# Optimization experiments

Hardware: AMD Instinct MI355X
Metric: run time of the kernel (lower is better)

Reference implementation:

```python
import jax, jax.numpy as jnp
import numpy as np

F_FIELDS = 39
VOCAB = 100000
EMB = 16
BATCH = 16384
H1, H2 = 32, 32


def setup_inputs() -> dict:
    key = jax.random.key(0)
    ks = jax.random.split(key, 10)
    Xi = jax.random.randint(ks[0], (BATCH, F_FIELDS, 1), 0, VOCAB, dtype=jnp.int64 if jax.config.jax_enable_x64 else jnp.int32).astype(jnp.int32)
    Xv = jax.random.uniform(ks[1], (BATCH, F_FIELDS), dtype=jnp.float32)
    # per-field embedding tables, stacked (all feature_sizes equal)
    emb1 = jax.random.normal(ks[2], (F_FIELDS, VOCAB, 1), dtype=jnp.float32)
    emb2 = jax.random.normal(ks[3], (F_FIELDS, VOCAB, EMB), dtype=jnp.float32)
    d_in = F_FIELDS * EMB
    W1 = jax.random.normal(ks[4], (d_in, H1), dtype=jnp.float32) / np.sqrt(d_in)
    b1 = jnp.zeros((H1,), dtype=jnp.float32)
    W2 = jax.random.normal(ks[5], (H1, H2), dtype=jnp.float32) / np.sqrt(H1)
    b2 = jnp.zeros((H2,), dtype=jnp.float32)
    bias = jax.random.normal(ks[6], (1,), dtype=jnp.float32)
    return {"Xi": Xi, "Xv": Xv, "emb1": emb1, "emb2": emb2,
            "W1": W1, "b1": b1, "W2": W2, "b2": b2, "bias": bias}


def reference(Xi, Xv, emb1, emb2, W1, b1, W2, b2, bias):
    B = Xi.shape[0]
    idx = Xi[:, :, 0]  # [B, F]
    # flatten per-field tables into one big table; offset indices by field
    off = idx + (jnp.arange(F_FIELDS, dtype=idx.dtype) * VOCAB)[None, :]  # [B, F]
    # first order: gather scalar per (b, f), scale by Xv
    first = emb1.reshape(F_FIELDS * VOCAB)[off] * Xv  # [B, F]
    # second order embeddings, scaled by Xv
    e2 = emb2.reshape(F_FIELDS * VOCAB, EMB)[off] * Xv[:, :, None]  # [B, F, E]
    s = jnp.sum(e2, axis=1)                      # [B, E]
    sq_sum = jnp.sum(e2 * e2, axis=1)            # [B, E]
    fm_second = 0.5 * (s * s - sq_sum)           # [B, E]
    # deep part on concatenated field embeddings
    deep_in = e2.reshape(B, F_FIELDS * EMB)
    h = jax.nn.relu(deep_in @ W1 + b1)
    h = jax.nn.relu(h @ W2 + b2)
    total = jnp.sum(first, axis=1) + jnp.sum(fm_second, axis=1) + jnp.sum(h, axis=1) + bias
    return total  # [B]
```

## Files before the change

kernel.cpp:

```cpp
#include <hip/hip_runtime.h>
#include <hip/hip_bf16.h>

#define F_FIELDS 39
#define VOCAB    100000
#define EMB      16
#define BATCH    16384
#define H1       32
#define H2       32
#define KSTEPS   20
#define KPW      5
#define FRAG_OFF (640*1024)

typedef __bf16 bf16x8 __attribute__((ext_vector_type(8)));
typedef float  f32x4  __attribute__((ext_vector_type(4)));

__global__ __launch_bounds__(256) void prep_kernel(
    const int*   __restrict__ Xi,  const float* __restrict__ Xv,
    const float* __restrict__ emb1,const float* __restrict__ W1,
    float* __restrict__ ws1, __bf16* __restrict__ wsfrag)
{
    const int blk = blockIdx.x;
    const int fld   = blk >> 5;
    const int chunk = blk & 31;
    const int t = threadIdx.x;
    const int b0 = chunk * 512 + t * 2;
    #pragma unroll
    for (int j = 0; j < 2; ++j) {
        int b = b0 + j;
        int idx  = Xi[b * F_FIELDS + fld];
        float xv = Xv[b * F_FIELDS + fld];
        ws1[b * F_FIELDS + fld] = emb1[fld * VOCAB + idx] * xv;
    }
    if (blk < 10) {
        int fidx = blk * 256 + t;
        if (fidx < KSTEPS * 2 * 64) {
            int lane = fidx & 63;
            int nh   = (fidx >> 6) & 1;
            int ks   = fidx >> 7;
            int k0   = ks * 32 + (lane >> 4) * 8;
            int n    = nh * 16 + (lane & 15);
            __bf16 vals[8];
            #pragma unroll
            for (int j = 0; j < 8; ++j) {
                int k = k0 + j;
                vals[j] = (k < F_FIELDS * EMB) ? (__bf16)W1[k * H1 + n] : (__bf16)0.0f;
            }
            *reinterpret_cast<bf16x8*>(&wsfrag[fidx * 8]) = *reinterpret_cast<const bf16x8*>(vals);
        }
    }
}

__global__ __launch_bounds__(256, 4) void deepfm_main(
    const int*   __restrict__ Xi,  const float* __restrict__ Xv,
    const float* __restrict__ emb2,
    const __bf16* __restrict__ wsW1, const float* __restrict__ ws1,
    const float* __restrict__ b1,  const float* __restrict__ W2,
    const float* __restrict__ b2,  const float* __restrict__ bias,
    float* __restrict__ out)
{
    __shared__ int   sXi[16 * F_FIELDS];
    __shared__ float sXv[16 * F_FIELDS];
    __shared__ float pacc[4][16][32];
    __shared__ float sbuf[4][16][16];
    __shared__ float qbuf[4][16];
    __shared__ float W2s[H1 * H2];
    __shared__ float hs[16][32];

    const int t    = threadIdx.x;
    const int h    = t >> 6;
    const int l    = t & 63;
    const int sloc = l & 15;
    const int q    = l >> 4;
    const int fpar = q >> 1;
    const int eoff = (q & 1) * 8;
    const int blk  = blockIdx.x;

    {
        const int base = blk * 16 * F_FIELDS;
        for (int i = t; i < 16 * F_FIELDS; i += 256) {
            sXi[i] = Xi[base + i];
            sXv[i] = Xv[base + i];
        }
    }
    reinterpret_cast<float4*>(W2s)[t] = reinterpret_cast<const float4*>(W2)[t];
    __syncthreads();

    float xvm[KPW];
    float4 g0[KPW], g1[KPW];
    #pragma unroll
    for (int ks = 0; ks < KPW; ++ks) {
        int f = 8 * ks + 2 * h + fpar;
        bool v = (f < F_FIELDS);
        int fi = v ? f : 0;
        int idx = sXi[sloc * F_FIELDS + fi];
        xvm[ks] = v ? sXv[sloc * F_FIELDS + fi] : 0.0f;
        const float4* rp = reinterpret_cast<const float4*>(emb2 + (fi * VOCAB + idx) * EMB + eoff);
        g0[ks] = rp[0];
        g1[ks] = rp[1];
    }

    const bf16x8* wsf = reinterpret_cast<const bf16x8*>(wsW1);
    f32x4 acc0 = {0.f,0.f,0.f,0.f}, acc1 = {0.f,0.f,0.f,0.f};
    float sa[8];
    float qq = 0.f;
    #pragma unroll
    for (int j = 0; j < 8; ++j) sa[j] = 0.f;

    #pragma unroll
    for (int ks = 0; ks < KPW; ++ks) {
        int kstep = 4 * ks + h;
        bf16x8 fr0 = wsf[(kstep * 2 + 0) * 64 + l];
        bf16x8 fr1 = wsf[(kstep * 2 + 1) * 64 + l];
        float xv = xvm[ks];
        float e[8] = { g0[ks].x*xv, g0[ks].y*xv, g0[ks].z*xv, g0[ks].w*xv,
                       g1[ks].x*xv, g1[ks].y*xv, g1[ks].z*xv, g1[ks].w*xv };
        bf16x8 a;
        #pragma unroll
        for (int j = 0; j < 8; ++j) {
            a[j] = (__bf16)e[j];
            sa[j] += e[j];
            qq   += e[j]*e[j];
        }
        acc0 = __builtin_amdgcn_mfma_f32_16x16x32_bf16(a, fr0, acc0, 0, 0, 0);
        acc1 = __builtin_amdgcn_mfma_f32_16x16x32_bf16(a, fr1, acc1, 0, 0, 0);
    }

    float sf[8];
    #pragma unroll
    for (int j = 0; j < 8; ++j) sf[j] = sa[j] + __shfl_xor(sa[j], 32);
    qq += __shfl_xor(qq, 32);
    qq += __shfl_xor(qq, 16);
    if (q < 2) {
        float4* srow = reinterpret_cast<float4*>(&sbuf[h][sloc][q * 8]);
        srow[0] = make_float4(sf[0], sf[1], sf[2], sf[3]);
        srow[1] = make_float4(sf[4], sf[5], sf[6], sf[7]);
    }
    if (l < 16) qbuf[h][sloc] = qq;

    float badd0 = (h == 0) ? b1[sloc]      : 0.f;
    float badd1 = (h == 0) ? b1[16 + sloc] : 0.f;
    #pragma unroll
    for (int r = 0; r < 4; ++r) {
        int row = q * 4 + r;
        pacc[h][row][sloc]      = acc0[r] + badd0;
        pacc[h][row][16 + sloc] = acc1[r] + badd1;
    }
    __syncthreads();

    {
        int ss = t >> 4, c = t & 15;
        hs[ss][c]      = fmaxf(pacc[0][ss][c]      + pacc[1][ss][c]      + pacc[2][ss][c]      + pacc[3][ss][c],      0.f);
        hs[ss][c + 16] = fmaxf(pacc[0][ss][c + 16] + pacc[1][ss][c + 16] + pacc[2][ss][c + 16] + pacc[3][ss][c + 16], 0.f);
    }
    __syncthreads();

    const int so = t >> 4;
    const int u  = t & 15;

    float sv = sbuf[0][so][u] + sbuf[1][so][u] + sbuf[2][so][u] + sbuf[3][so][u];
    float s2 = sv * sv;

    const float* w1row = ws1 + (blk * 16 + so) * F_FIELDS;
    float fo = w1row[u] + w1row[16 + u];
    if (u < 7) fo += w1row[32 + u];

    float a0 = b2[2 * u], a1 = b2[2 * u + 1];
    #pragma unroll
    for (int i = 0; i < H1; ++i) {
        float hv = hs[so][i];
        a0 += hv * W2s[i * H2 + 2 * u];
        a1 += hv * W2s[i * H2 + 2 * u + 1];
    }
    float psum = fmaxf(a0, 0.f) + fmaxf(a1, 0.f) + fo;

    psum += __shfl_xor(psum, 1);  s2 += __shfl_xor(s2, 1);
    psum += __shfl_xor(psum, 2);  s2 += __shfl_xor(s2, 2);
    psum += __shfl_xor(psum, 4);  s2 += __shfl_xor(s2, 4);
    psum += __shfl_xor(psum, 8);  s2 += __shfl_xor(s2, 8);

    if (u == 0) {
        float qtot = qbuf[0][so] + qbuf[1][so] + qbuf[2][so] + qbuf[3][so];
        out[blk * 16 + so] = psum + 0.5f * (s2 - qtot) + bias[0];
    }
}

extern "C" void kernel_launch(void* const* d_in, const int* in_sizes, int n_in,
                              void* d_out, int out_size, void* d_ws, size_t ws_size,
                              hipStream_t stream) {
    const int*   Xi   = (const int*)  d_in[0];
    const float* Xv   = (const float*)d_in[1];
    const float* emb1 = (const float*)d_in[2];
    const float* emb2 = (const float*)d_in[3];
    const float* W1   = (const float*)d_in[4];
    const float* b1   = (const float*)d_in[5];
    const float* W2   = (const float*)d_in[6];
    const float* b2   = (const float*)d_in[7];
    const float* bias = (const float*)d_in[8];
    float* out = (float*)d_out;

    float*  ws1    = (float*)d_ws;
    __bf16* wsfrag = (__bf16*)((float*)d_ws + FRAG_OFF);

    prep_kernel<<<F_FIELDS * 32, 256, 0, stream>>>(Xi, Xv, emb1, W1, ws1, wsfrag);
    deepfm_main<<<BATCH/16, 256, 0, stream>>>(Xi, Xv, emb2, wsfrag, ws1, b1, W2, b2, bias, out);
}
```

Before: 36.05 us.

## Transpose Xi field-major and split prep into separate emb1 gather kernels

Splits the old prep kernel into three: a W1 bf16 fragment swizzle, a shared-memory transpose of Xi into field-major order, and an emb1 gather that reads and writes coalesced field-major arrays. The Xv multiply for the first-order term moves into the main kernel, which reads the field-major gathered values. The aim is coalesced index reads and output writes, with blocks grouped by field for locality in the emb1 table. This adds two extra kernel launches and an extra global round trip for the transposed Xi, and the main kernel's first-order reads become strided across fields.

After: 37.48 us. 4.0% more time.

```diff
diff --git a/kernel.cpp b/kernel.cpp
--- a/kernel.cpp
+++ b/kernel.cpp
@@ -9,51 +9,73 @@
 #define H2       32
 #define KSTEPS   20
 #define KPW      5
-#define FRAG_OFF (640*1024)
+
+#define WS1E_OFF  0
+#define XIT_OFF   2555904
+#define FRAG_OFF  5111808
 
 typedef __bf16 bf16x8 __attribute__((ext_vector_type(8)));
 typedef float  f32x4  __attribute__((ext_vector_type(4)));
 
-__global__ __launch_bounds__(256) void prep_kernel(
-    const int*   __restrict__ Xi,  const float* __restrict__ Xv,
-    const float* __restrict__ emb1,const float* __restrict__ W1,
-    float* __restrict__ ws1, __bf16* __restrict__ wsfrag)
-{
+__global__ __launch_bounds__(256) void swizzle_w1_kernel(const float* __restrict__ W1,
+                                                         __bf16* __restrict__ ws)
+{
+    int fidx = blockIdx.x * 256 + threadIdx.x;
+    if (fidx >= KSTEPS * 2 * 64) return;
+    int lane = fidx & 63;
+    int nh   = (fidx >> 6) & 1;
+    int ks   = fidx >> 7;
+    int k0   = ks * 32 + (lane >> 4) * 8;
+    int n    = nh * 16 + (lane & 15);
+    __bf16 vals[8];
+    #pragma unroll
+    for (int j = 0; j < 8; ++j) {
+        int k = k0 + j;
+        vals[j] = (k < F_FIELDS * EMB) ? (__bf16)W1[k * H1 + n] : (__bf16)0.0f;
+    }
+    *reinterpret_cast<bf16x8*>(&ws[fidx * 8]) = *reinterpret_cast<const bf16x8*>(vals);
+}
+
+__global__ __launch_bounds__(256) void xi_transpose_kernel(const int* __restrict__ Xi,
+                                                           int* __restrict__ XiT)
+{
+    __shared__ int tile[F_FIELDS][65];
     const int blk = blockIdx.x;
-    const int fld   = blk >> 5;
-    const int chunk = blk & 31;
-    const int t = threadIdx.x;
-    const int b0 = chunk * 512 + t * 2;
-    #pragma unroll
-    for (int j = 0; j < 2; ++j) {
-        int b = b0 + j;
-        int idx  = Xi[b * F_FIELDS + fld];
-        float xv = Xv[b * F_FIELDS + fld];
-        ws1[b * F_FIELDS + fld] = emb1[fld * VOCAB + idx] * xv;
-    }
-    if (blk < 10) {
-        int fidx = blk * 256 + t;
-        if (fidx < KSTEPS * 2 * 64) {
-            int lane = fidx & 63;
-            int nh   = (fidx >> 6) & 1;
-            int ks   = fidx >> 7;
-            int k0   = ks * 32 + (lane >> 4) * 8;
-            int n    = nh * 16 + (lane & 15);
-            __bf16 vals[8];
-            #pragma unroll
-            for (int j = 0; j < 8; ++j) {
-                int k = k0 + j;
-                vals[j] = (k < F_FIELDS * EMB) ? (__bf16)W1[k * H1 + n] : (__bf16)0.0f;
-            }
-            *reinterpret_cast<bf16x8*>(&wsfrag[fidx * 8]) = *reinterpret_cast<const bf16x8*>(vals);
-        }
-    }
+    const int t   = threadIdx.x;
+    const int base = blk * 64 * F_FIELDS;
+    for (int i = t; i < 64 * F_FIELDS; i += 256) {
+        int s = i / F_FIELDS, f = i % F_FIELDS;
+        tile[f][s] = Xi[base + i];
+    }
+    __syncthreads();
+    for (int j = t; j < 64 * F_FIELDS; j += 256) {
+        int f = j >> 6, s = j & 63;
+        XiT[f * BATCH + blk * 64 + s] = tile[f][s];
+    }
+}
+
+__global__ __launch_bounds__(256) void emb1_prep_kernel(const int* __restrict__ XiT,
+                                                        const float* __restrict__ emb1,
+                                                        float* __restrict__ ws1e)
+{
+    const int b     = blockIdx.x;
+    const int sgrp  = b >> 3;
+    const int field = (b & 7) + 8 * (sgrp >> 5);
+    if (field >= F_FIELDS) return;
+    const int chunk = sgrp & 31;
+    const int g = chunk * 512 + threadIdx.x * 2;
+    int2 idx = *reinterpret_cast<const int2*>(&XiT[field * BATCH + g]);
+    const float* eb = emb1 + (size_t)field * VOCAB;
+    float2 o;
+    o.x = eb[idx.x];
+    o.y = eb[idx.y];
+    *reinterpret_cast<float2*>(&ws1e[field * BATCH + g]) = o;
 }
 
 __global__ __launch_bounds__(256, 4) void deepfm_main(
     const int*   __restrict__ Xi,  const float* __restrict__ Xv,
     const float* __restrict__ emb2,
-    const __bf16* __restrict__ wsW1, const float* __restrict__ ws1,
+    const __bf16* __restrict__ wsW1, const float* __restrict__ ws1e,
     const float* __restrict__ b1,  const float* __restrict__ W2,
     const float* __restrict__ b2,  const float* __restrict__ bias,
     float* __restrict__ out)
@@ -156,13 +178,15 @@
 
     const int so = t >> 4;
     const int u  = t & 15;
+    const int sg = blk * 16 + so;
 
     float sv = sbuf[0][so][u] + sbuf[1][so][u] + sbuf[2][so][u] + sbuf[3][so][u];
     float s2 = sv * sv;
 
-    const float* w1row = ws1 + (blk * 16 + so) * F_FIELDS;
-    float fo = w1row[u] + w1row[16 + u];
-    if (u < 7) fo += w1row[32 + u];
+    float fo = ws1e[u * BATCH + sg]        * sXv[so * F_FIELDS + u]
+             + ws1e[(u + 16) * BATCH + sg] * sXv[so * F_FIELDS + u + 16];
+    if (u < 7)
+        fo += ws1e[(u + 32) * BATCH + sg] * sXv[so * F_FIELDS + u + 32];
 
     float a0 = b2[2 * u], a1 = b2[2 * u + 1];
     #pragma unroll
@@ -180,7 +204,7 @@
 
     if (u == 0) {
         float qtot = qbuf[0][so] + qbuf[1][so] + qbuf[2][so] + qbuf[3][so];
-        out[blk * 16 + so] = psum + 0.5f * (s2 - qtot) + bias[0];
+        out[sg] = psum + 0.5f * (s2 - qtot) + bias[0];
     }
 }
 
@@ -198,9 +222,13 @@
     const float* bias = (const float*)d_in[8];
     float* out = (float*)d_out;
 
-    float*  ws1    = (float*)d_ws;
-    __bf16* wsfrag = (__bf16*)((float*)d_ws + FRAG_OFF);
-
-    prep_kernel<<<F_FIELDS * 32, 256, 0, stream>>>(Xi, Xv, emb1, W1, ws1, wsfrag);
-    deepfm_main<<<BATCH/16, 256, 0, stream>>>(Xi, Xv, emb2, wsfrag, ws1, b1, W2, b2, bias, out);
-}
+    char* wsb = (char*)d_ws;
+    float*  ws1e   = (float*)(wsb + WS1E_OFF);
+    int*    XiT    = (int*)  (wsb + XIT_OFF);
+    __bf16* wsfrag = (__bf16*)(wsb + FRAG_OFF);
+
+    swizzle_w1_kernel<<<(KSTEPS*2*64 + 255)/256, 256, 0, stream>>>(W1, wsfrag);
+    xi_transpose_kernel<<<BATCH/64, 256, 0, stream>>>(Xi, XiT);
+    emb1_prep_kernel<<<1280, 256, 0, stream>>>(XiT, emb1, ws1e);
+    deepfm_main<<<BATCH/16, 256, 0, stream>>>(Xi, Xv, emb2, wsfrag, ws1e, b1, W2, b2, bias, out);
+}
```
